# Kernel tuning notes

Hardware: AMD Instinct MI355X
Metric: run time of the kernel (lower is better)

The kernel has to match this reference:

```python
import jax, jax.numpy as jnp
import numpy as np

N_MEMBERS = 2      # ensemble_length=3, loop runs i=1..2
N_NODES = 65536    # batch_size * total_length = 32 * 2048
N_EDGES = 1_048_576
N_LAYERS = 12      # num_conv_layers
D = 64             # constant feature width (linspace 64->64)


def setup_inputs() -> dict:
    key = jax.random.key(0)
    k0, k1, k2, k3 = jax.random.split(key, 4)
    x = jax.random.normal(k0, (N_MEMBERS, N_NODES, D), dtype=jnp.float32)
    edge_index = jax.random.randint(k1, (N_MEMBERS, 2, N_EDGES), 0, N_NODES, dtype=jnp.int64)
    # GCNConv weights per member/layer; scale ~ 1/sqrt(D) for stability across 12 layers
    W = jax.random.normal(k2, (N_MEMBERS, N_LAYERS, D, D), dtype=jnp.float32) / jnp.sqrt(jnp.float32(D))
    b = jax.random.normal(k3, (N_MEMBERS, N_LAYERS, D), dtype=jnp.float32) * 0.01
    return {"x": x, "edge_index": edge_index, "W": W, "b": b}


def gcn_conv(h, src, dst, W, b):
    """PyG GCNConv: add self-loops, symmetric D^-1/2 (A+I) D^-1/2 normalization,
    linear transform, bias."""
    hw = h @ W                                                # [N, D_out]
    # degree includes the self-loop (+1)
    deg = jax.ops.segment_sum(jnp.ones((src.shape[0],), h.dtype), dst,
                              num_segments=N_NODES) + jnp.asarray(1.0, h.dtype)
    dinv = jax.lax.rsqrt(deg)                                 # [N]
    norm = dinv[src] * dinv[dst]                              # [E]
    agg = jax.ops.segment_sum(norm[:, None] * hw[src], dst, num_segments=N_NODES)
    agg = agg + (dinv * dinv)[:, None] * hw                   # self-loop term
    return agg + b


def reference(x, edge_index, W, b):
    # eval mode: F.dropout(training=False) is identity
    outs = []
    for i in range(N_MEMBERS):
        src, dst = edge_index[i, 0], edge_index[i, 1]
        h = x[i]
        for j in range(N_LAYERS - 1):
            h = jax.nn.relu(gcn_conv(h, src, dst, W[i, j], b[i, j]))
        outs.append(gcn_conv(h, src, dst, W[i, N_LAYERS - 1], b[i, N_LAYERS - 1]))
    return jnp.stack(outs)  # [N_MEMBERS, N_NODES, D]
```

## Files before the change

### kernel.cpp

```cpp
#include <hip/hip_runtime.h>
#include <hip/hip_fp16.h>
#include <math.h>

#define N_MEMBERS 2
#define N_NODES   65536
#define N_EDGES   1048576
#define N_LAYERS  12
#define D         64
#define OFF_STRIDE (N_NODES + 1)
#define NODE_MASK (N_NODES - 1)

#define NBINS       256
#define BIN_CAP     5120
#define EDGES_PER_WG 4096

typedef _Float16 f16;
typedef f16   f16x8 __attribute__((ext_vector_type(8)));
typedef float f32x4 __attribute__((ext_vector_type(4)));


__global__ __launch_bounds__(256) void bin_scatter_k(const int* __restrict__ ei,
                                                     int* __restrict__ binCursor,
                                                     unsigned int* __restrict__ binned) {
    int m = blockIdx.y;
    int t = threadIdx.x;
    int eBase = blockIdx.x * EDGES_PER_WG;
    __shared__ int hist[NBINS];
    __shared__ int base[NBINS];
    hist[t] = 0;
    __syncthreads();
    const int* srcp = ei + (size_t)(m * 2 + 0) * N_EDGES;
    const int* dstp = ei + (size_t)(m * 2 + 1) * N_EDGES;
    unsigned int pk[16];
    int bn[16], rk[16];
    #pragma unroll
    for (int i = 0; i < 16; i++) {
        int e = eBase + i * 256 + t;
        int src = srcp[e] & NODE_MASK;
        int dst = dstp[e] & NODE_MASK;
        int b = dst >> 8;
        bn[i] = b;
        pk[i] = ((unsigned)src << 8) | (unsigned)(dst & 255);
        rk[i] = atomicAdd(&hist[b], 1);
    }
    __syncthreads();
    base[t] = atomicAdd(&binCursor[m * NBINS + t], hist[t]);
    __syncthreads();
    unsigned int* bb = binned + (size_t)m * NBINS * BIN_CAP;
    #pragma unroll
    for (int i = 0; i < 16; i++) {
        int pos = base[bn[i]] + rk[i];
        if (pos < BIN_CAP)
            bb[(size_t)bn[i] * BIN_CAP + pos] = pk[i];
    }
}

__global__ __launch_bounds__(256) void scan_bins_k(const int* __restrict__ cur,
                                                   int* __restrict__ bbase) {
    int m = blockIdx.x, t = threadIdx.x;
    __shared__ int sh[256];
    int v0 = cur[m * NBINS + t];
    sh[t] = v0;
    __syncthreads();
    for (int ofs = 1; ofs < 256; ofs <<= 1) {
        int v = sh[t];
        int a = (t >= ofs) ? sh[t - ofs] : 0;
        __syncthreads();
        sh[t] = v + a;
        __syncthreads();
    }
    bbase[m * NBINS + t] = sh[t] - v0;
}

__global__ __launch_bounds__(256) void bin_build_k(const unsigned int* __restrict__ binned,
                                                   const int* __restrict__ binCursor,
                                                   const int* __restrict__ bbase,
                                                   int* __restrict__ off,
                                                   float* __restrict__ dinv,
                                                   unsigned short* __restrict__ csr_src) {
    int m = blockIdx.y, b = blockIdx.x, t = threadIdx.x;
    int cnt   = binCursor[m * NBINS + b];
    int gbase = bbase[m * NBINS + b];
    const unsigned int* bb = binned + ((size_t)m * NBINS + b) * BIN_CAP;
    __shared__ int degl[256];
    __shared__ int offl[256];
    degl[t] = 0;
    __syncthreads();
    unsigned int ed[20];
    #pragma unroll
    for (int j = 0; j < 20; j++) {
        int i = t + j * 256;
        ed[j] = 0;
        if (i < cnt) {
            unsigned int w = bb[i];
            int r = atomicAdd(&degl[w & 255], 1);
            ed[j] = w | ((unsigned)r << 24);
        }
    }
    __syncthreads();
    int myDeg = degl[t];
    offl[t] = myDeg;
    __syncthreads();
    for (int ofs = 1; ofs < 256; ofs <<= 1) {
        int v = offl[t];
        int a = (t >= ofs) ? offl[t - ofs] : 0;
        __syncthreads();
        offl[t] = v + a;
        __syncthreads();
    }
    int myOff = gbase + offl[t] - myDeg;
    int node = b * 256 + t;
    off[m * OFF_STRIDE + node] = myOff;
    if (b == NBINS - 1 && t == 255) off[m * OFF_STRIDE + N_NODES] = N_EDGES;
    dinv[m * N_NODES + node] = 1.0f / sqrtf((float)myDeg + 1.0f);
    offl[t] = myOff;
    __syncthreads();
    unsigned short* cs = csr_src + (size_t)m * N_EDGES;
    #pragma unroll
    for (int j = 0; j < 20; j++) {
        int i = t + j * 256;
        if (i < cnt) {
            int dl  = ed[j] & 255;
            int src = (ed[j] >> 8) & 0xFFFF;
            int r   = ed[j] >> 24;
            cs[offl[dl] + r] = (unsigned short)src;
        }
    }
}

__device__ __forceinline__ void split8(const float* p, f16x8& hi, f16x8& lo) {
    float4 a = *(const float4*)p;
    float4 b = *(const float4*)(p + 4);
    float v[8] = {a.x, a.y, a.z, a.w, b.x, b.y, b.z, b.w};
    #pragma unroll
    for (int i = 0; i < 8; i++) {
        f16 h = (f16)v[i];
        hi[i] = h;
        lo[i] = (f16)(v[i] - (float)h);
    }
}

__global__ __launch_bounds__(256) void gemm_mfma_k(const float* __restrict__ h,
                                                   const float* __restrict__ Wall,
                                                   const float* __restrict__ dinv,
                                                   __half* __restrict__ hw, int layer) {
    int m = blockIdx.y;
    const float* Wg = Wall + (size_t)(m * N_LAYERS + layer) * D * D;
    __shared__ __align__(16) _Float16 Whi[D][72];
    __shared__ __align__(16) _Float16 Wlo[D][72];
    for (int idx = threadIdx.x; idx < D * D / 4; idx += 256) {
        float4 v = ((const float4*)Wg)[idx];
        int k  = idx >> 4;
        int c0 = (idx & 15) << 2;
        float vv[4] = {v.x, v.y, v.z, v.w};
        #pragma unroll
        for (int i = 0; i < 4; i++) {
            f16 hi = (f16)vv[i];
            Whi[c0 + i][k] = hi;
            Wlo[c0 + i][k] = (f16)(vv[i] - (float)hi);
        }
    }
    __syncthreads();

    int lane = threadIdx.x & 63;
    int wav  = threadIdx.x >> 6;
    int nn   = lane & 15;
    int quad = lane >> 4;

    f16x8 Bh[8], Bl[8];
    #pragma unroll
    for (int t = 0; t < 4; t++)
        #pragma unroll
        for (int s = 0; s < 2; s++) {
            Bh[t * 2 + s] = *(const f16x8*)&Whi[t * 16 + nn][s * 32 + quad * 8];
            Bl[t * 2 + s] = *(const f16x8*)&Wlo[t * 16 + nn][s * 32 + quad * 8];
        }

    const float* hm = h + (size_t)m * N_NODES * D;
    const float* dm = dinv + m * N_NODES;
    __half*      om = hw + (size_t)m * N_NODES * D;
    int base = blockIdx.x * 256 + wav * 64;
    for (int g = 0; g < 4; g++) {
        int n0 = base + g * 16;
        const float* hrow = hm + (size_t)(n0 + nn) * D;
        f16x8 ah[2], al[2];
        split8(hrow + quad * 8,      ah[0], al[0]);
        split8(hrow + 32 + quad * 8, ah[1], al[1]);
        float dvr[4];
        #pragma unroll
        for (int r = 0; r < 4; r++) dvr[r] = dm[n0 + quad * 4 + r];
        #pragma unroll
        for (int t = 0; t < 4; t++) {
            f32x4 c = {0.f, 0.f, 0.f, 0.f};
            #pragma unroll
            for (int s = 0; s < 2; s++) {
                c = __builtin_amdgcn_mfma_f32_16x16x32_f16(ah[s], Bh[t*2+s], c, 0, 0, 0);
                c = __builtin_amdgcn_mfma_f32_16x16x32_f16(al[s], Bh[t*2+s], c, 0, 0, 0);
                c = __builtin_amdgcn_mfma_f32_16x16x32_f16(ah[s], Bl[t*2+s], c, 0, 0, 0);
            }
            #pragma unroll
            for (int r = 0; r < 4; r++)
                om[(size_t)(n0 + quad * 4 + r) * D + t * 16 + nn] =
                    __float2half((float)c[r] * dvr[r]);
        }
    }
}

__device__ __forceinline__ void cvt8(uint4 u, float* f) {
    const __half2* h2 = (const __half2*)&u;
    #pragma unroll
    for (int i = 0; i < 4; i++) {
        float2 t = __half22float2(h2[i]);
        f[2 * i]     = t.x;
        f[2 * i + 1] = t.y;
    }
}

__global__ __launch_bounds__(256) void aggregate_k(const __half* __restrict__ hw,
                                                   float* __restrict__ out,
                                                   const int* __restrict__ off,
                                                   const unsigned short* __restrict__ csr_src,
                                                   const float* __restrict__ dinv,
                                                   const float* __restrict__ ball,
                                                   int layer, int relu) {
    int m = blockIdx.y;
    int n = blockIdx.x * 4 + (threadIdx.x >> 6);
    int lane = threadIdx.x & 63;
    int fg   = lane & 7;
    int sub  = lane >> 3;
    const __half*         hm = hw + (size_t)m * N_NODES * D;
    const int*            ob = off + m * OFF_STRIDE;
    const unsigned short* sb = csr_src + (size_t)m * N_EDGES;

    float acc[8];
    #pragma unroll
    for (int i = 0; i < 8; i++) acc[i] = 0.f;

    int e0 = ob[n], e1 = ob[n + 1];
    #pragma unroll 2
    for (int e = e0; e < e1; e += 8) {
        int ee  = e + sub;
        int idx = (ee < e1) ? ee : (e1 - 1);
        int s   = sb[idx];
        float w = (ee < e1) ? 1.0f : 0.0f;
        uint4 g = *(const uint4*)(hm + (size_t)s * D + fg * 8);
        float f[8];
        cvt8(g, f);
        #pragma unroll
        for (int i = 0; i < 8; i++) acc[i] = fmaf(w, f[i], acc[i]);
    }
    #pragma unroll
    for (int msk = 8; msk < 64; msk <<= 1)
        #pragma unroll
        for (int i = 0; i < 8; i++) acc[i] += __shfl_xor(acc[i], msk);

    float dv = dinv[m * N_NODES + n];
    uint4 sg = *(const uint4*)(hm + (size_t)n * D + fg * 8);
    float sf[8];
    cvt8(sg, sf);
    const float* bp = ball + (size_t)(m * N_LAYERS + layer) * D + fg * 8;
    #pragma unroll
    for (int i = 0; i < 8; i++) {
        acc[i] = fmaf(dv, acc[i] + sf[i], bp[i]);
        if (relu) acc[i] = fmaxf(acc[i], 0.f);
    }
    if (sub == 0) {
        float4* op = (float4*)(out + (size_t)m * N_NODES * D + (size_t)n * D + fg * 8);
        op[0] = make_float4(acc[0], acc[1], acc[2], acc[3]);
        op[1] = make_float4(acc[4], acc[5], acc[6], acc[7]);
    }
}


extern "C" void kernel_launch(void* const* d_in, const int* in_sizes, int n_in,
                              void* d_out, int out_size, void* d_ws, size_t ws_size,
                              hipStream_t stream) {
    (void)in_sizes; (void)n_in; (void)out_size; (void)ws_size;
    const float* x  = (const float*)d_in[0];
    const int*   ei = (const int*)d_in[1];
    const float* W  = (const float*)d_in[2];
    const float* b  = (const float*)d_in[3];
    float* out = (float*)d_out;

    char* ws = (char*)d_ws;
    size_t o = 0;
    auto take = [&](size_t bytes) -> void* {
        void* p = ws + o;
        o = (o + bytes + 255) & ~(size_t)255;
        return p;
    };
    float*          dinv      = (float*) take((size_t)N_MEMBERS * N_NODES * 4);
    int*            off       = (int*)   take((size_t)N_MEMBERS * OFF_STRIDE * 4);
    int*            binCursor = (int*)   take((size_t)N_MEMBERS * NBINS * 4);
    int*            bbase     = (int*)   take((size_t)N_MEMBERS * NBINS * 4);
    unsigned short* csr_src   = (unsigned short*)take((size_t)N_MEMBERS * N_EDGES * 2);
    __half*         tbuf      = (__half*)take((size_t)N_MEMBERS * N_NODES * D * 2);
    float*          hbuf      = (float*) take((size_t)N_MEMBERS * N_NODES * D * 4);
    unsigned int*   binned    = (unsigned int*)hbuf;

    hipMemsetAsync(binCursor, 0, (size_t)N_MEMBERS * NBINS * 4, stream);

    bin_scatter_k<<<dim3(N_EDGES / EDGES_PER_WG, N_MEMBERS), 256, 0, stream>>>(
        ei, binCursor, binned);
    scan_bins_k<<<dim3(N_MEMBERS), 256, 0, stream>>>(binCursor, bbase);
    bin_build_k<<<dim3(NBINS, N_MEMBERS), 256, 0, stream>>>(
        binned, binCursor, bbase, off, dinv, csr_src);

    const float* hin = x;
    for (int j = 0; j < N_LAYERS; j++) {
        gemm_mfma_k<<<dim3(N_NODES / 256, N_MEMBERS), 256, 0, stream>>>(hin, W, dinv, tbuf, j);
        float* dst = (j == N_LAYERS - 1) ? out : hbuf;
        aggregate_k<<<dim3(N_NODES / 4, N_MEMBERS), 256, 0, stream>>>(
            tbuf, dst, off, csr_src, dinv, b, j, (j < N_LAYERS - 1) ? 1 : 0);
        hin = hbuf;
    }
}
```

Measured before the change: 911.3 us.

## Aggregate before transform and keep all intermediate activations in fp16

After: 915.1 us. Within noise of the previous version (+0.4%).

```diff
diff --git a/kernel.cpp b/kernel.cpp
--- a/kernel.cpp
+++ b/kernel.cpp
@@ -128,22 +128,88 @@
     }
 }
 
-__device__ __forceinline__ void split8(const float* p, f16x8& hi, f16x8& lo) {
-    float4 a = *(const float4*)p;
-    float4 b = *(const float4*)(p + 4);
-    float v[8] = {a.x, a.y, a.z, a.w, b.x, b.y, b.z, b.w};
-    #pragma unroll
-    for (int i = 0; i < 8; i++) {
-        f16 h = (f16)v[i];
-        hi[i] = h;
-        lo[i] = (f16)(v[i] - (float)h);
-    }
-}
-
-__global__ __launch_bounds__(256) void gemm_mfma_k(const float* __restrict__ h,
-                                                   const float* __restrict__ Wall,
-                                                   const float* __restrict__ dinv,
-                                                   __half* __restrict__ hw, int layer) {
+__global__ __launch_bounds__(256) void prescale_k(const float* __restrict__ x,
+                                                  const float* __restrict__ dinv,
+                                                  __half* __restrict__ g) {
+    int i = blockIdx.x * 256 + threadIdx.x;
+    float dv = dinv[i >> 3];
+    float4 a = ((const float4*)x)[i * 2];
+    float4 b = ((const float4*)x)[i * 2 + 1];
+    union { __half2 h2[4]; uint4 u; } p;
+    p.h2[0] = __floats2half2_rn(dv * a.x, dv * a.y);
+    p.h2[1] = __floats2half2_rn(dv * a.z, dv * a.w);
+    p.h2[2] = __floats2half2_rn(dv * b.x, dv * b.y);
+    p.h2[3] = __floats2half2_rn(dv * b.z, dv * b.w);
+    ((uint4*)g)[i] = p.u;
+}
+
+__device__ __forceinline__ void cvt8(uint4 u, float* f) {
+    const __half2* h2 = (const __half2*)&u;
+    #pragma unroll
+    for (int i = 0; i < 4; i++) {
+        float2 t = __half22float2(h2[i]);
+        f[2 * i]     = t.x;
+        f[2 * i + 1] = t.y;
+    }
+}
+
+__global__ __launch_bounds__(256) void aggregate_k(const __half* __restrict__ g,
+                                                   __half* __restrict__ S,
+                                                   const int* __restrict__ off,
+                                                   const unsigned short* __restrict__ csr_src,
+                                                   const float* __restrict__ dinv) {
+    int m = blockIdx.y;
+    int n = blockIdx.x * 4 + (threadIdx.x >> 6);
+    int lane = threadIdx.x & 63;
+    int fg   = lane & 7;
+    int sub  = lane >> 3;
+    const __half*         gm = g + (size_t)m * N_NODES * D;
+    const int*            ob = off + m * OFF_STRIDE;
+    const unsigned short* sb = csr_src + (size_t)m * N_EDGES;
+
+    float acc[8];
+    #pragma unroll
+    for (int i = 0; i < 8; i++) acc[i] = 0.f;
+
+    int e0 = ob[n], e1 = ob[n + 1];
+    #pragma unroll 2
+    for (int e = e0; e < e1; e += 8) {
+        int ee  = e + sub;
+        int idx = (ee < e1) ? ee : (e1 - 1);
+        int s   = sb[idx];
+        float w = (ee < e1) ? 1.0f : 0.0f;
+        uint4 gv = *(const uint4*)(gm + (size_t)s * D + fg * 8);
+        float f[8];
+        cvt8(gv, f);
+        #pragma unroll
+        for (int i = 0; i < 8; i++) acc[i] = fmaf(w, f[i], acc[i]);
+    }
+    #pragma unroll
+    for (int msk = 8; msk < 64; msk <<= 1)
+        #pragma unroll
+        for (int i = 0; i < 8; i++) acc[i] += __shfl_xor(acc[i], msk);
+
+    float dv = dinv[m * N_NODES + n];
+    uint4 sg = *(const uint4*)(gm + (size_t)n * D + fg * 8);
+    float sf[8];
+    cvt8(sg, sf);
+    if (sub == 0) {
+        union { __half2 h2[4]; uint4 u; } p;
+        #pragma unroll
+        for (int i = 0; i < 4; i++)
+            p.h2[i] = __floats2half2_rn(dv * (acc[2 * i]     + sf[2 * i]),
+                                        dv * (acc[2 * i + 1] + sf[2 * i + 1]));
+        *(uint4*)(S + (size_t)m * N_NODES * D + (size_t)n * D + fg * 8) = p.u;
+    }
+}
+
+__global__ __launch_bounds__(256) void gemm_f16_k(const __half* __restrict__ S,
+                                                  const float* __restrict__ Wall,
+                                                  const float* __restrict__ dinv,
+                                                  const float* __restrict__ ball,
+                                                  __half* __restrict__ gout,
+                                                  float* __restrict__ fout,
+                                                  int layer, int last) {
     int m = blockIdx.y;
     const float* Wg = Wall + (size_t)(m * N_LAYERS + layer) * D * D;
     __shared__ __align__(16) _Float16 Whi[D][72];
@@ -176,98 +242,44 @@
             Bl[t * 2 + s] = *(const f16x8*)&Wlo[t * 16 + nn][s * 32 + quad * 8];
         }
 
-    const float* hm = h + (size_t)m * N_NODES * D;
-    const float* dm = dinv + m * N_NODES;
-    __half*      om = hw + (size_t)m * N_NODES * D;
+    const __half* Sm = S + (size_t)m * N_NODES * D;
+    const float*  dm = dinv + m * N_NODES;
+    const float*  bp = ball + (size_t)(m * N_LAYERS + layer) * D;
+    __half*       gm = gout + (size_t)m * N_NODES * D;
+    float*        fm = fout + (size_t)m * N_NODES * D;
+
+    float bcol[4];
+    #pragma unroll
+    for (int t = 0; t < 4; t++) bcol[t] = bp[t * 16 + nn];
+
     int base = blockIdx.x * 256 + wav * 64;
     for (int g = 0; g < 4; g++) {
         int n0 = base + g * 16;
-        const float* hrow = hm + (size_t)(n0 + nn) * D;
-        f16x8 ah[2], al[2];
-        split8(hrow + quad * 8,      ah[0], al[0]);
-        split8(hrow + 32 + quad * 8, ah[1], al[1]);
+        const __half* srow = Sm + (size_t)(n0 + nn) * D;
+        f16x8 a0 = *(const f16x8*)(srow + quad * 8);
+        f16x8 a1 = *(const f16x8*)(srow + 32 + quad * 8);
         float dvr[4];
         #pragma unroll
         for (int r = 0; r < 4; r++) dvr[r] = dm[n0 + quad * 4 + r];
         #pragma unroll
         for (int t = 0; t < 4; t++) {
             f32x4 c = {0.f, 0.f, 0.f, 0.f};
+            c = __builtin_amdgcn_mfma_f32_16x16x32_f16(a0, Bh[t * 2 + 0], c, 0, 0, 0);
+            c = __builtin_amdgcn_mfma_f32_16x16x32_f16(a1, Bh[t * 2 + 1], c, 0, 0, 0);
+            c = __builtin_amdgcn_mfma_f32_16x16x32_f16(a0, Bl[t * 2 + 0], c, 0, 0, 0);
+            c = __builtin_amdgcn_mfma_f32_16x16x32_f16(a1, Bl[t * 2 + 1], c, 0, 0, 0);
             #pragma unroll
-            for (int s = 0; s < 2; s++) {
-                c = __builtin_amdgcn_mfma_f32_16x16x32_f16(ah[s], Bh[t*2+s], c, 0, 0, 0);
-                c = __builtin_amdgcn_mfma_f32_16x16x32_f16(al[s], Bh[t*2+s], c, 0, 0, 0);
-                c = __builtin_amdgcn_mfma_f32_16x16x32_f16(ah[s], Bl[t*2+s], c, 0, 0, 0);
+            for (int r = 0; r < 4; r++) {
+                int row = n0 + quad * 4 + r;
+                float v = (float)c[r] + bcol[t];
+                if (last) {
+                    fm[(size_t)row * D + t * 16 + nn] = v;
+                } else {
+                    gm[(size_t)row * D + t * 16 + nn] =
+                        __float2half(fmaxf(v, 0.f) * dvr[r]);
+                }
             }
-            #pragma unroll
-            for (int r = 0; r < 4; r++)
-                om[(size_t)(n0 + quad * 4 + r) * D + t * 16 + nn] =
-                    __float2half((float)c[r] * dvr[r]);
-        }
-    }
-}
-
-__device__ __forceinline__ void cvt8(uint4 u, float* f) {
-    const __half2* h2 = (const __half2*)&u;
-    #pragma unroll
-    for (int i = 0; i < 4; i++) {
-        float2 t = __half22float2(h2[i]);
-        f[2 * i]     = t.x;
-        f[2 * i + 1] = t.y;
-    }
-}
-
-__global__ __launch_bounds__(256) void aggregate_k(const __half* __restrict__ hw,
-                                                   float* __restrict__ out,
-                                                   const int* __restrict__ off,
-                                                   const unsigned short* __restrict__ csr_src,
-                                                   const float* __restrict__ dinv,
-                                                   const float* __restrict__ ball,
-                                                   int layer, int relu) {
-    int m = blockIdx.y;
-    int n = blockIdx.x * 4 + (threadIdx.x >> 6);
-    int lane = threadIdx.x & 63;
-    int fg   = lane & 7;
-    int sub  = lane >> 3;
-    const __half*         hm = hw + (size_t)m * N_NODES * D;
-    const int*            ob = off + m * OFF_STRIDE;
-    const unsigned short* sb = csr_src + (size_t)m * N_EDGES;
-
-    float acc[8];
-    #pragma unroll
-    for (int i = 0; i < 8; i++) acc[i] = 0.f;
-
-    int e0 = ob[n], e1 = ob[n + 1];
-    #pragma unroll 2
-    for (int e = e0; e < e1; e += 8) {
-        int ee  = e + sub;
-        int idx = (ee < e1) ? ee : (e1 - 1);
-        int s   = sb[idx];
-        float w = (ee < e1) ? 1.0f : 0.0f;
-        uint4 g = *(const uint4*)(hm + (size_t)s * D + fg * 8);
-        float f[8];
-        cvt8(g, f);
-        #pragma unroll
-        for (int i = 0; i < 8; i++) acc[i] = fmaf(w, f[i], acc[i]);
-    }
-    #pragma unroll
-    for (int msk = 8; msk < 64; msk <<= 1)
-        #pragma unroll
-        for (int i = 0; i < 8; i++) acc[i] += __shfl_xor(acc[i], msk);
-
-    float dv = dinv[m * N_NODES + n];
-    uint4 sg = *(const uint4*)(hm + (size_t)n * D + fg * 8);
-    float sf[8];
-    cvt8(sg, sf);
-    const float* bp = ball + (size_t)(m * N_LAYERS + layer) * D + fg * 8;
-    #pragma unroll
-    for (int i = 0; i < 8; i++) {
-        acc[i] = fmaf(dv, acc[i] + sf[i], bp[i]);
-        if (relu) acc[i] = fmaxf(acc[i], 0.f);
-    }
-    if (sub == 0) {
-        float4* op = (float4*)(out + (size_t)m * N_NODES * D + (size_t)n * D + fg * 8);
-        op[0] = make_float4(acc[0], acc[1], acc[2], acc[3]);
-        op[1] = make_float4(acc[4], acc[5], acc[6], acc[7]);
+        }
     }
 }
 
@@ -294,9 +306,9 @@
     int*            binCursor = (int*)   take((size_t)N_MEMBERS * NBINS * 4);
     int*            bbase     = (int*)   take((size_t)N_MEMBERS * NBINS * 4);
     unsigned short* csr_src   = (unsigned short*)take((size_t)N_MEMBERS * N_EDGES * 2);
-    __half*         tbuf      = (__half*)take((size_t)N_MEMBERS * N_NODES * D * 2);
-    float*          hbuf      = (float*) take((size_t)N_MEMBERS * N_NODES * D * 4);
-    unsigned int*   binned    = (unsigned int*)hbuf;
+    __half*         gbuf      = (__half*)take((size_t)N_MEMBERS * N_NODES * D * 2);
+    __half*         Sbuf      = (__half*)take((size_t)N_MEMBERS * N_NODES * D * 2);
+    unsigned int*   binned    = (unsigned int*)Sbuf;
 
     hipMemsetAsync(binCursor, 0, (size_t)N_MEMBERS * NBINS * 4, stream);
 
@@ -305,13 +317,13 @@
     scan_bins_k<<<dim3(N_MEMBERS), 256, 0, stream>>>(binCursor, bbase);
     bin_build_k<<<dim3(NBINS, N_MEMBERS), 256, 0, stream>>>(
         binned, binCursor, bbase, off, dinv, csr_src);
-
-    const float* hin = x;
+    prescale_k<<<dim3((N_MEMBERS * N_NODES * D / 8) / 256), 256, 0, stream>>>(
+        x, dinv, gbuf);
+
     for (int j = 0; j < N_LAYERS; j++) {
-        gemm_mfma_k<<<dim3(N_NODES / 256, N_MEMBERS), 256, 0, stream>>>(hin, W, dinv, tbuf, j);
-        float* dst = (j == N_LAYERS - 1) ? out : hbuf;
         aggregate_k<<<dim3(N_NODES / 4, N_MEMBERS), 256, 0, stream>>>(
-            tbuf, dst, off, csr_src, dinv, b, j, (j < N_LAYERS - 1) ? 1 : 0);
-        hin = hbuf;
-    }
-}
+            gbuf, Sbuf, off, csr_src, dinv);
+        gemm_f16_k<<<dim3(N_NODES / 256, N_MEMBERS), 256, 0, stream>>>(
+            Sbuf, W, dinv, b, gbuf, out, j, (j == N_LAYERS - 1) ? 1 : 0);
+    }
+}
```
